# Optimization experiments

Measured on AMD Instinct MI355X. Metric: run time of the kernel, lower is better.

The kernel has to match this reference:

```python
import jax, jax.numpy as jnp
import numpy as np

B_SZ, L, H, P = 4, 4096, 1024, 1024
R_MIN, R_MAX, MAX_PHASE = 0.0, 1.0, 6.28


def setup_inputs() -> dict:
    key = jax.random.key(0)
    ks = jax.random.split(key, 8)
    inputs = jax.random.normal(ks[0], (B_SZ, L, H), dtype=jnp.float32)
    # LRU-style init for nu_log/theta_log (keeps |lambda| < 1 so scan is stable)
    u1 = jax.random.uniform(ks[1], (P,))
    nu = -0.5 * jnp.log(u1 * (R_MAX**2 - R_MIN**2) + R_MIN**2)
    nu_log = jnp.log(nu)
    u2 = jax.random.uniform(ks[2], (P,))
    theta_log = jnp.log(MAX_PHASE * u2)
    # variance_scaling(0.5,'fan_out','normal') for B; (1.0,'fan_out','normal') for C
    B_re = jax.random.normal(ks[3], (P, H)) * jnp.sqrt(0.5 / P)
    B_im = jax.random.normal(ks[4], (P, H)) * jnp.sqrt(0.5 / P)
    C_re = jax.random.normal(ks[5], (H, P)) * jnp.sqrt(1.0 / H)
    C_im = jax.random.normal(ks[6], (H, P)) * jnp.sqrt(1.0 / H)
    D = jax.random.normal(ks[7], (H,))
    diag_lambda = jnp.exp(-jnp.exp(nu_log) + 1j * jnp.exp(theta_log))
    gamma_log = jnp.log(jnp.sqrt(1.0 - jnp.abs(diag_lambda) ** 2))
    return {
        "inputs": inputs,
        "nu_log": nu_log.astype(jnp.float32),
        "theta_log": theta_log.astype(jnp.float32),
        "B_re": B_re.astype(jnp.float32),
        "B_im": B_im.astype(jnp.float32),
        "C_re": C_re.astype(jnp.float32),
        "C_im": C_im.astype(jnp.float32),
        "D": D.astype(jnp.float32),
        "gamma_log": gamma_log.astype(jnp.float32),
    }


def reference(inputs, nu_log, theta_log, B_re, B_im, C_re, C_im, D, gamma_log):
    batch_size, input_length, _ = inputs.shape
    Lambda = jnp.exp(-jnp.exp(nu_log) + 1j * jnp.exp(theta_log))  # [P] complex
    Bmat = B_re + 1j * B_im                                        # [P,H]
    Cmat = C_re + 1j * C_im                                        # [H,P]
    gamma = jnp.exp(gamma_log)                                     # [P]
    B_norm = Bmat * gamma[:, None]

    def apply_step(elem_i, elem_j):
        a_i, bu_i = elem_i
        a_j, bu_j = elem_j
        return (a_j * a_i, a_j * bu_i + bu_j)

    Ls = jnp.broadcast_to(Lambda, (batch_size, input_length, Lambda.shape[0]))
    Bu = jnp.einsum('ph,blh->blp', B_norm, inputs.astype(B_norm.dtype))
    _, xs = jax.lax.associative_scan(apply_step, (Ls, Bu), axis=1)
    Cx = jnp.einsum('hp,blp->blh', Cmat, xs).real
    Du = D * inputs
    return Cx + Du
```

## Files before the change

### kernel.cpp

```cpp
#include <hip/hip_runtime.h>
#include <cstdint>
#include <cstddef>

#define MDIM 16384
#define HDIM 1024
#define PDIM 1024
#define LSEQ 4096
#define BSZ  4
#define CHUNK 64
#define NCHUNK 64
#define NBU  2048

typedef float   floatx4  __attribute__((ext_vector_type(4)));
typedef __bf16  bf16x8   __attribute__((ext_vector_type(8)));
typedef unsigned short u16;
typedef unsigned short u16x8 __attribute__((ext_vector_type(8)));

__device__ __forceinline__ u16 f2bf(float f) {
    union { float f; uint32_t u; } v; v.f = f;
    return (u16)((v.u + 0x7fffu + ((v.u >> 16) & 1u)) >> 16);
}
__device__ __forceinline__ float bfu2f(uint32_t bits16) {
    union { float f; uint32_t u; } v; v.u = bits16 << 16; return v.f;
}
__device__ __forceinline__ bf16x8 ldfrag(const u16* p) {
    return __builtin_bit_cast(bf16x8, *(const u16x8*)p);
}
__device__ __forceinline__ void gload16(const u16* g, u16* l) {
    __builtin_amdgcn_global_load_lds(
        (const __attribute__((address_space(1))) uint32_t*)g,
        (__attribute__((address_space(3))) uint32_t*)l, 16, 0, 0);
}

template<int KD>
__device__ __forceinline__ void gemm_core(
    const u16* __restrict__ A, const u16* __restrict__ B,
    int m0, int n0, u16* sA, u16* sB, floatx4 acc[4][4])
{
    const int tid  = threadIdx.x;
    const int wave = tid >> 6, lane = tid & 63;
    const int lrow = lane & 15, lq = lane >> 4;
    const int wm = (wave >> 1) * 64, wn = (wave & 1) * 64;
    const int srow   = lane >> 3;
    const int schunk = (lane & 7) ^ srow;

    const u16* aptr = A + (size_t)(m0 + wave * 32 + srow) * KD + schunk * 8;
    const u16* bptr = B + (size_t)(n0 + wave * 32 + srow) * KD + schunk * 8;
    u16* sAw = sA + wave * 32 * 64;
    u16* sBw = sB + wave * 32 * 64;

    for (int k0 = 0; k0 < KD; k0 += 64) {
        #pragma unroll
        for (int i = 0; i < 4; ++i) {
            gload16(aptr + (size_t)i * 8 * KD + k0, sAw + i * 8 * 64);
            gload16(bptr + (size_t)i * 8 * KD + k0, sBw + i * 8 * 64);
        }
        __syncthreads();
        #pragma unroll
        for (int s = 0; s < 2; ++s) {
            bf16x8 af[4], bfr[4];
            #pragma unroll
            for (int mt = 0; mt < 4; ++mt) {
                int r = wm + mt * 16 + lrow;
                af[mt] = ldfrag(sA + r * 64 + (((s * 4 + lq) ^ (r & 7)) * 8));
            }
            #pragma unroll
            for (int nt = 0; nt < 4; ++nt) {
                int r = wn + nt * 16 + lrow;
                bfr[nt] = ldfrag(sB + r * 64 + (((s * 4 + lq) ^ (r & 7)) * 8));
            }
            #pragma unroll
            for (int mt = 0; mt < 4; ++mt)
                #pragma unroll
                for (int nt = 0; nt < 4; ++nt)
                    acc[mt][nt] = __builtin_amdgcn_mfma_f32_16x16x32_bf16(
                        af[mt], bfr[nt], acc[mt][nt], 0, 0, 0);
        }
        __syncthreads();
    }
}

#define ST 136
__global__ __launch_bounds__(256) void gemm_bu_k(
    const u16* __restrict__ A, const u16* __restrict__ B, u16* __restrict__ O)
{
    __shared__ u16 smem[128 * ST];
    u16* sA = smem;
    u16* sB = smem + 128 * 64;
    floatx4 acc[4][4] = {};
    const int n0 = blockIdx.x * 128, m0 = blockIdx.y * 128;
    gemm_core<HDIM>(A, B, m0, n0, sA, sB, acc);

    const int tid = threadIdx.x, wave = tid >> 6, lane = tid & 63;
    const int lrow = lane & 15, lq = lane >> 4;
    const int wm = (wave >> 1) * 64, wn = (wave & 1) * 64;

    #pragma unroll
    for (int nt = 0; nt < 4; ++nt) {
        int col = wn + nt * 16 + lrow;
        #pragma unroll
        for (int mt = 0; mt < 4; ++mt)
            #pragma unroll
            for (int r = 0; r < 4; ++r) {
                int row = wm + mt * 16 + lq * 4 + r;
                smem[row * ST + col] = f2bf(acc[mt][nt][r]);
            }
    }
    __syncthreads();

    const int col = (tid & 15) * 8;
    const int rb  = tid >> 4;
    #pragma unroll
    for (int j = 0; j < 8; ++j) {
        int row = rb + j * 16;
        *(u16x8*)(O + (size_t)(m0 + row) * NBU + n0 + col) =
            *(const u16x8*)(smem + row * ST + col);
    }
}

__global__ __launch_bounds__(256) void gemm_out_k(
    const u16* __restrict__ A, const u16* __restrict__ B,
    const float* __restrict__ Dv, const u16* __restrict__ Ubf,
    float* __restrict__ O)
{
    __shared__ u16 sA[128 * 64];
    __shared__ u16 sB[128 * 64];
    floatx4 acc[4][4] = {};
    const int n0 = blockIdx.x * 128, m0 = blockIdx.y * 128;
    gemm_core<NBU>(A, B, m0, n0, sA, sB, acc);

    const int tid = threadIdx.x, wave = tid >> 6, lane = tid & 63;
    const int lrow = lane & 15, lq = lane >> 4;
    const int wm = (wave >> 1) * 64, wn = (wave & 1) * 64;
    #pragma unroll
    for (int nt = 0; nt < 4; ++nt) {
        int col = n0 + wn + nt * 16 + lrow;
        float d = Dv[col];
        #pragma unroll
        for (int mt = 0; mt < 4; ++mt)
            #pragma unroll
            for (int r = 0; r < 4; ++r) {
                int row = m0 + wm + mt * 16 + lq * 4 + r;
                size_t o = (size_t)row * HDIM + col;
                O[o] = acc[mt][nt][r] + d * bfu2f(Ubf[o]);
            }
    }
}

__global__ __launch_bounds__(256) void cvt_u_bf(
    const float* __restrict__ in, u16* __restrict__ out)
{
    size_t i = ((size_t)blockIdx.x * 256 + threadIdx.x) * 8;
    float4 a = *(const float4*)(in + i);
    float4 b = *(const float4*)(in + i + 4);
    u16x8 w;
    w[0]=f2bf(a.x); w[1]=f2bf(a.y); w[2]=f2bf(a.z); w[3]=f2bf(a.w);
    w[4]=f2bf(b.x); w[5]=f2bf(b.y); w[6]=f2bf(b.z); w[7]=f2bf(b.w);
    *(u16x8*)(out + i) = w;
}

__global__ __launch_bounds__(256) void prep_bcomb(
    const float* __restrict__ Bre, const float* __restrict__ Bim,
    const float* __restrict__ gamma_log, u16* __restrict__ out)
{
    int t = blockIdx.x * 256 + threadIdx.x;
    int n = t >> 7;
    int h = (t & 127) * 8;
    int p = n >> 1, s = n & 1;
    const float* src = (s ? Bim : Bre) + (size_t)p * HDIM + h;
    float g = expf(gamma_log[p]);
    float4 a = *(const float4*)src;
    float4 b = *(const float4*)(src + 4);
    u16x8 w;
    w[0]=f2bf(a.x*g); w[1]=f2bf(a.y*g); w[2]=f2bf(a.z*g); w[3]=f2bf(a.w*g);
    w[4]=f2bf(b.x*g); w[5]=f2bf(b.y*g); w[6]=f2bf(b.z*g); w[7]=f2bf(b.w*g);
    *(u16x8*)(out + (size_t)n * HDIM + h) = w;
}

__global__ __launch_bounds__(256) void prep_bc(
    const float* __restrict__ Cre, const float* __restrict__ Cim,
    u16* __restrict__ out)
{
    int t = blockIdx.x * 256 + threadIdx.x;
    int h = t >> 8;
    int k = (t & 255) * 4;
    float4 cr = *(const float4*)(Cre + (size_t)h * PDIM + k);
    float4 ci = *(const float4*)(Cim + (size_t)h * PDIM + k);
    u16x8 w;
    w[0]=f2bf(cr.x); w[1]=f2bf(-ci.x);
    w[2]=f2bf(cr.y); w[3]=f2bf(-ci.y);
    w[4]=f2bf(cr.z); w[5]=f2bf(-ci.z);
    w[6]=f2bf(cr.w); w[7]=f2bf(-ci.w);
    *(u16x8*)(out + (size_t)h * NBU + 2 * k) = w;
}

__global__ __launch_bounds__(256) void scan_passA(
    const uint32_t* __restrict__ BuC,
    const float* __restrict__ nu_log, const float* __restrict__ theta_log,
    float* __restrict__ endC)
{
    int tid = blockIdx.x * 256 + threadIdx.x;
    int p0 = (tid & 511) * 2;
    int c  = (tid >> 9) & (NCHUNK - 1);
    int b  = tid >> 15;
    float nu0 = expf(nu_log[p0]),     th0 = expf(theta_log[p0]);
    float nu1 = expf(nu_log[p0 + 1]), th1 = expf(theta_log[p0 + 1]);
    float el0 = expf(-nu0), el1 = expf(-nu1);
    float lr0 = el0 * cosf(th0), li0 = el0 * sinf(th0);
    float lr1 = el1 * cosf(th1), li1 = el1 * sinf(th1);
    const uint32_t* src = BuC + (size_t)(b * LSEQ + c * CHUNK) * PDIM + p0;
    float xr0 = 0.f, xi0 = 0.f, xr1 = 0.f, xi1 = 0.f;
    #pragma unroll 8
    for (int t = 0; t < CHUNK; ++t) {
        uint2 v = *(const uint2*)(src + (size_t)t * PDIM);
        float br0 = bfu2f(v.x & 0xffffu), bi0 = bfu2f(v.x >> 16);
        float br1 = bfu2f(v.y & 0xffffu), bi1 = bfu2f(v.y >> 16);
        float nr0 = fmaf(lr0, xr0, fmaf(-li0, xi0, br0));
        float ni0 = fmaf(lr0, xi0, fmaf(li0, xr0, bi0));
        float nr1 = fmaf(lr1, xr1, fmaf(-li1, xi1, br1));
        float ni1 = fmaf(lr1, xi1, fmaf(li1, xr1, bi1));
        xr0 = nr0; xi0 = ni0; xr1 = nr1; xi1 = ni1;
    }
    float4 e; e.x = xr0; e.y = xi0; e.z = xr1; e.w = xi1;
    *(float4*)(endC + (((size_t)b * NCHUNK + c) * PDIM + p0) * 2) = e;
}

__global__ __launch_bounds__(256) void scan_passB(
    const float* __restrict__ endC,
    const float* __restrict__ nu_log, const float* __restrict__ theta_log,
    float* __restrict__ carryC)
{
    int tid = blockIdx.x * 256 + threadIdx.x;
    int p0 = (tid & 511) * 2;
    int b  = tid >> 9;
    float nu0 = expf(nu_log[p0]),     th0 = expf(theta_log[p0]);
    float nu1 = expf(nu_log[p0 + 1]), th1 = expf(theta_log[p0 + 1]);
    float e0 = expf(-nu0 * (float)CHUNK), a0 = th0 * (float)CHUNK;
    float e1 = expf(-nu1 * (float)CHUNK), a1 = th1 * (float)CHUNK;
    float Lr0 = e0 * cosf(a0), Li0 = e0 * sinf(a0);
    float Lr1 = e1 * cosf(a1), Li1 = e1 * sinf(a1);
    float gr0 = 0.f, gi0 = 0.f, gr1 = 0.f, gi1 = 0.f;
    for (int g = 0; g < 8; ++g) {
        float4 e[8];
        #pragma unroll
        for (int j = 0; j < 8; ++j)
            e[j] = *(const float4*)(endC + (((size_t)b * NCHUNK + g * 8 + j) * PDIM + p0) * 2);
        #pragma unroll
        for (int j = 0; j < 8; ++j) {
            size_t idx = (((size_t)b * NCHUNK + g * 8 + j) * PDIM + p0) * 2;
            float4 go; go.x = gr0; go.y = gi0; go.z = gr1; go.w = gi1;
            *(float4*)(carryC + idx) = go;
            float nr0 = fmaf(Lr0, gr0, fmaf(-Li0, gi0, e[j].x));
            float ni0 = fmaf(Lr0, gi0, fmaf(Li0, gr0, e[j].y));
            float nr1 = fmaf(Lr1, gr1, fmaf(-Li1, gi1, e[j].z));
            float ni1 = fmaf(Lr1, gi1, fmaf(Li1, gr1, e[j].w));
            gr0 = nr0; gi0 = ni0; gr1 = nr1; gi1 = ni1;
        }
    }
}

__global__ __launch_bounds__(256) void scan_passC(
    uint32_t* __restrict__ BuC,
    const float* __restrict__ nu_log, const float* __restrict__ theta_log,
    const float* __restrict__ carryC)
{
    int tid = blockIdx.x * 256 + threadIdx.x;
    int p0 = (tid & 511) * 2;
    int c  = (tid >> 9) & (NCHUNK - 1);
    int b  = tid >> 15;
    float nu0 = expf(nu_log[p0]),     th0 = expf(theta_log[p0]);
    float nu1 = expf(nu_log[p0 + 1]), th1 = expf(theta_log[p0 + 1]);
    float el0 = expf(-nu0), el1 = expf(-nu1);
    float lr0 = el0 * cosf(th0), li0 = el0 * sinf(th0);
    float lr1 = el1 * cosf(th1), li1 = el1 * sinf(th1);
    float4 g = *(const float4*)(carryC + (((size_t)b * NCHUNK + c) * PDIM + p0) * 2);
    float xr0 = g.x, xi0 = g.y, xr1 = g.z, xi1 = g.w;
    uint32_t* ptr = BuC + (size_t)(b * LSEQ + c * CHUNK) * PDIM + p0;
    #pragma unroll 8
    for (int t = 0; t < CHUNK; ++t) {
        uint32_t* q = ptr + (size_t)t * PDIM;
        uint2 v = *(const uint2*)q;
        float br0 = bfu2f(v.x & 0xffffu), bi0 = bfu2f(v.x >> 16);
        float br1 = bfu2f(v.y & 0xffffu), bi1 = bfu2f(v.y >> 16);
        float nr0 = fmaf(lr0, xr0, fmaf(-li0, xi0, br0));
        float ni0 = fmaf(lr0, xi0, fmaf(li0, xr0, bi0));
        float nr1 = fmaf(lr1, xr1, fmaf(-li1, xi1, br1));
        float ni1 = fmaf(lr1, xi1, fmaf(li1, xr1, bi1));
        xr0 = nr0; xi0 = ni0; xr1 = nr1; xi1 = ni1;
        uint2 o;
        o.x = (uint32_t)f2bf(xr0) | ((uint32_t)f2bf(xi0) << 16);
        o.y = (uint32_t)f2bf(xr1) | ((uint32_t)f2bf(xi1) << 16);
        *(uint2*)q = o;
    }
}

extern "C" void kernel_launch(void* const* d_in, const int* in_sizes, int n_in,
                              void* d_out, int out_size, void* d_ws, size_t ws_size,
                              hipStream_t stream)
{
    (void)in_sizes; (void)n_in; (void)out_size; (void)ws_size;
    const float* U         = (const float*)d_in[0];
    const float* nu_log    = (const float*)d_in[1];
    const float* theta_log = (const float*)d_in[2];
    const float* B_re      = (const float*)d_in[3];
    const float* B_im      = (const float*)d_in[4];
    const float* C_re      = (const float*)d_in[5];
    const float* C_im      = (const float*)d_in[6];
    const float* Dv        = (const float*)d_in[7];
    const float* gamma_log = (const float*)d_in[8];
    float* out = (float*)d_out;

    char* ws = (char*)d_ws;
    u16*   BuC    = (u16*)ws;
    u16*   Ubf    = (u16*)(ws + (size_t)64 * 1024 * 1024);
    u16*   Bcomb  = (u16*)(ws + (size_t)96 * 1024 * 1024);
    u16*   Bcbf   = (u16*)(ws + (size_t)100 * 1024 * 1024);
    float* endC   = (float*)(ws + (size_t)104 * 1024 * 1024);
    float* carryC = (float*)(ws + (size_t)106 * 1024 * 1024);

    cvt_u_bf  <<<(MDIM * HDIM) / (256 * 8), 256, 0, stream>>>(U, Ubf);
    prep_bcomb<<<(NBU * HDIM) / (256 * 8), 256, 0, stream>>>(B_re, B_im, gamma_log, Bcomb);
    prep_bc   <<<(HDIM * PDIM) / (256 * 4), 256, 0, stream>>>(C_re, C_im, Bcbf);

    dim3 g1(NBU / 128, MDIM / 128);
    gemm_bu_k<<<g1, 256, 0, stream>>>(Ubf, Bcomb, BuC);

    scan_passA<<<(BSZ * NCHUNK * PDIM / 2) / 256, 256, 0, stream>>>(
        (const uint32_t*)BuC, nu_log, theta_log, endC);
    scan_passB<<<(BSZ * PDIM / 2) / 256, 256, 0, stream>>>(endC, nu_log, theta_log, carryC);
    scan_passC<<<(BSZ * NCHUNK * PDIM / 2) / 256, 256, 0, stream>>>(
        (uint32_t*)BuC, nu_log, theta_log, carryC);

    dim3 g3(HDIM / 128, MDIM / 128);
    gemm_out_k<<<g3, 256, 0, stream>>>(BuC, Bcbf, Dv, Ubf, out);
}
```

Baseline: 357.0 us.

## Remap GEMM blocks per XCD for L2 locality and fuse prep kernels

Both GEMM kernels switch to a 1D grid whose block index is remapped so that consecutive blocks landing on the same XCD (assuming round-robin dispatch across 8 XCDs) share contiguous row panels of A. Each XCD's private L2 then holds the A tiles its own blocks reuse. The three prep kernels (input conversion to bf16, B scaling and packing, C packing) are merged into one launch that branches on block index, removing two launches. The mapping relies on an assumed dispatch order and on hardcoded grid sizes.

```diff
diff --git a/kernel.cpp b/kernel.cpp
--- a/kernel.cpp
+++ b/kernel.cpp
@@ -88,7 +88,10 @@
     u16* sA = smem;
     u16* sB = smem + 128 * 64;
     floatx4 acc[4][4] = {};
-    const int n0 = blockIdx.x * 128, m0 = blockIdx.y * 128;
+    const int d = blockIdx.x;
+    const int xcd = d & 7, s = d >> 3;
+    const int m0 = (xcd * 16 + (s >> 4)) * 128;
+    const int n0 = (s & 15) * 128;
     gemm_core<HDIM>(A, B, m0, n0, sA, sB, acc);
 
     const int tid = threadIdx.x, wave = tid >> 6, lane = tid & 63;
@@ -126,7 +129,10 @@
     __shared__ u16 sA[128 * 64];
     __shared__ u16 sB[128 * 64];
     floatx4 acc[4][4] = {};
-    const int n0 = blockIdx.x * 128, m0 = blockIdx.y * 128;
+    const int d = blockIdx.x;
+    const int xcd = d & 7, s = d >> 3;
+    const int m0 = (xcd * 16 + (s >> 3)) * 128;
+    const int n0 = (s & 7) * 128;
     gemm_core<NBU>(A, B, m0, n0, sA, sB, acc);
 
     const int tid = threadIdx.x, wave = tid >> 6, lane = tid & 63;
@@ -135,63 +141,60 @@
     #pragma unroll
     for (int nt = 0; nt < 4; ++nt) {
         int col = n0 + wn + nt * 16 + lrow;
-        float d = Dv[col];
+        float dval = Dv[col];
         #pragma unroll
         for (int mt = 0; mt < 4; ++mt)
             #pragma unroll
             for (int r = 0; r < 4; ++r) {
                 int row = m0 + wm + mt * 16 + lq * 4 + r;
                 size_t o = (size_t)row * HDIM + col;
-                O[o] = acc[mt][nt][r] + d * bfu2f(Ubf[o]);
+                O[o] = acc[mt][nt][r] + dval * bfu2f(Ubf[o]);
             }
     }
 }
 
-__global__ __launch_bounds__(256) void cvt_u_bf(
-    const float* __restrict__ in, u16* __restrict__ out)
-{
-    size_t i = ((size_t)blockIdx.x * 256 + threadIdx.x) * 8;
-    float4 a = *(const float4*)(in + i);
-    float4 b = *(const float4*)(in + i + 4);
-    u16x8 w;
-    w[0]=f2bf(a.x); w[1]=f2bf(a.y); w[2]=f2bf(a.z); w[3]=f2bf(a.w);
-    w[4]=f2bf(b.x); w[5]=f2bf(b.y); w[6]=f2bf(b.z); w[7]=f2bf(b.w);
-    *(u16x8*)(out + i) = w;
-}
-
-__global__ __launch_bounds__(256) void prep_bcomb(
+__global__ __launch_bounds__(256) void prep_all(
+    const float* __restrict__ U, u16* __restrict__ Ubf,
     const float* __restrict__ Bre, const float* __restrict__ Bim,
-    const float* __restrict__ gamma_log, u16* __restrict__ out)
-{
-    int t = blockIdx.x * 256 + threadIdx.x;
-    int n = t >> 7;
-    int h = (t & 127) * 8;
-    int p = n >> 1, s = n & 1;
-    const float* src = (s ? Bim : Bre) + (size_t)p * HDIM + h;
-    float g = expf(gamma_log[p]);
-    float4 a = *(const float4*)src;
-    float4 b = *(const float4*)(src + 4);
-    u16x8 w;
-    w[0]=f2bf(a.x*g); w[1]=f2bf(a.y*g); w[2]=f2bf(a.z*g); w[3]=f2bf(a.w*g);
-    w[4]=f2bf(b.x*g); w[5]=f2bf(b.y*g); w[6]=f2bf(b.z*g); w[7]=f2bf(b.w*g);
-    *(u16x8*)(out + (size_t)n * HDIM + h) = w;
-}
-
-__global__ __launch_bounds__(256) void prep_bc(
+    const float* __restrict__ gamma_log, u16* __restrict__ Bcomb,
     const float* __restrict__ Cre, const float* __restrict__ Cim,
-    u16* __restrict__ out)
-{
-    int t = blockIdx.x * 256 + threadIdx.x;
-    int h = t >> 8;
-    int k = (t & 255) * 4;
-    float4 cr = *(const float4*)(Cre + (size_t)h * PDIM + k);
-    float4 ci = *(const float4*)(Cim + (size_t)h * PDIM + k);
-    u16x8 w;
-    w[0]=f2bf(cr.x); w[1]=f2bf(-ci.x);
-    w[2]=f2bf(cr.y); w[3]=f2bf(-ci.y);
-    w[4]=f2bf(cr.z); w[5]=f2bf(-ci.z);
-    w[6]=f2bf(cr.w); w[7]=f2bf(-ci.w);
-    *(u16x8*)(out + (size_t)h * NBU + 2 * k) = w;
+    u16* __restrict__ Bcbf)
+{
+    const int bid = blockIdx.x;
+    if (bid < 8192) {
+        size_t i = ((size_t)bid * 256 + threadIdx.x) * 8;
+        float4 a = *(const float4*)(U + i);
+        float4 b = *(const float4*)(U + i + 4);
+        u16x8 w;
+        w[0]=f2bf(a.x); w[1]=f2bf(a.y); w[2]=f2bf(a.z); w[3]=f2bf(a.w);
+        w[4]=f2bf(b.x); w[5]=f2bf(b.y); w[6]=f2bf(b.z); w[7]=f2bf(b.w);
+        *(u16x8*)(Ubf + i) = w;
+    } else if (bid < 9216) {
+        int t = (bid - 8192) * 256 + threadIdx.x;
+        int n = t >> 7;
+        int h = (t & 127) * 8;
+        int p = n >> 1, sflag = n & 1;
+        const float* src = (sflag ? Bim : Bre) + (size_t)p * HDIM + h;
+        float g = expf(gamma_log[p]);
+        float4 a = *(const float4*)src;
+        float4 b = *(const float4*)(src + 4);
+        u16x8 w;
+        w[0]=f2bf(a.x*g); w[1]=f2bf(a.y*g); w[2]=f2bf(a.z*g); w[3]=f2bf(a.w*g);
+        w[4]=f2bf(b.x*g); w[5]=f2bf(b.y*g); w[6]=f2bf(b.z*g); w[7]=f2bf(b.w*g);
+        *(u16x8*)(Bcomb + (size_t)n * HDIM + h) = w;
+    } else {
+        int t = (bid - 9216) * 256 + threadIdx.x;
+        int h = t >> 8;
+        int k = (t & 255) * 4;
+        float4 cr = *(const float4*)(Cre + (size_t)h * PDIM + k);
+        float4 ci = *(const float4*)(Cim + (size_t)h * PDIM + k);
+        u16x8 w;
+        w[0]=f2bf(cr.x); w[1]=f2bf(-ci.x);
+        w[2]=f2bf(cr.y); w[3]=f2bf(-ci.y);
+        w[4]=f2bf(cr.z); w[5]=f2bf(-ci.z);
+        w[6]=f2bf(cr.w); w[7]=f2bf(-ci.w);
+        *(u16x8*)(Bcbf + (size_t)h * NBU + 2 * k) = w;
+    }
 }
 
 __global__ __launch_bounds__(256) void scan_passA(
@@ -318,12 +321,10 @@
     float* endC   = (float*)(ws + (size_t)104 * 1024 * 1024);
     float* carryC = (float*)(ws + (size_t)106 * 1024 * 1024);
 
-    cvt_u_bf  <<<(MDIM * HDIM) / (256 * 8), 256, 0, stream>>>(U, Ubf);
-    prep_bcomb<<<(NBU * HDIM) / (256 * 8), 256, 0, stream>>>(B_re, B_im, gamma_log, Bcomb);
-    prep_bc   <<<(HDIM * PDIM) / (256 * 4), 256, 0, stream>>>(C_re, C_im, Bcbf);
-
-    dim3 g1(NBU / 128, MDIM / 128);
-    gemm_bu_k<<<g1, 256, 0, stream>>>(Ubf, Bcomb, BuC);
+    prep_all<<<8192 + 1024 + 1024, 256, 0, stream>>>(
+        U, Ubf, B_re, B_im, gamma_log, Bcomb, C_re, C_im, Bcbf);
+
+    gemm_bu_k<<<2048, 256, 0, stream>>>(Ubf, Bcomb, BuC);
 
     scan_passA<<<(BSZ * NCHUNK * PDIM / 2) / 256, 256, 0, stream>>>(
         (const uint32_t*)BuC, nu_log, theta_log, endC);
@@ -331,6 +332,5 @@
     scan_passC<<<(BSZ * NCHUNK * PDIM / 2) / 256, 256, 0, stream>>>(
         (uint32_t*)BuC, nu_log, theta_log, carryC);
 
-    dim3 g3(HDIM / 128, MDIM / 128);
-    gemm_out_k<<<g3, 256, 0, stream>>>(BuC, Bcbf, Dv, Ubf, out);
-}
+    gemm_out_k<<<1024, 256, 0, stream>>>(BuC, Bcbf, Dv, Ubf, out);
+}
```

Result: faster. 327.6 us (-8.2%).
